# Optimization experiments

Hardware: AMD Instinct MI355X
Metric: run time of the kernel (lower is better)

Reference implementation:

```python
import jax, jax.numpy as jnp
import numpy as np

K, D = 8, 4
LOG2PI = float(np.log(2.0 * np.pi))
TRIL_ROWS, TRIL_COLS = np.tril_indices(D)


def setup_inputs() -> dict:
    key = jax.random.key(0)
    k1, k2 = jax.random.split(key)
    M = 512
    B = 4096
    phi_dim = K + K * D + K * D * (D + 1) // 2  # 120
    phi = jax.random.normal(k1, (M, phi_dim), dtype=jnp.float32)
    X_ref = jax.random.normal(k2, (B, D), dtype=jnp.float32)
    return {"phi": phi, "X_ref": X_ref}


def reference(phi, X_ref):
    M = phi.shape[0]
    B = X_ref.shape[0]
    # unpack_phi: [pi_tilde | mu | L_vecs]
    pi_tilde = phi[:, :K]                                   # [M, K]
    mu = phi[:, K:K + K * D].reshape(M, K, D)               # [M, K, D]
    L_vecs = phi[:, K + K * D:].reshape(M, K, D * (D + 1) // 2)
    # L_vec_to_matrix: lower-triangular fill (row-major tril order)
    L = jnp.zeros((M, K, D, D), phi.dtype).at[:, :, TRIL_ROWS, TRIL_COLS].set(L_vecs)
    pi = jax.nn.softmax(pi_tilde, axis=-1)                  # [M, K]

    # --- mean responsibilities (GMM E-step) ---
    diff = X_ref[None, None, :, :] - mu[:, :, None, :]      # [M, K, B, D]
    L_flat = L.reshape(M * K, D, D)
    diff_flat = jnp.transpose(diff.reshape(M * K, B, D), (0, 2, 1))  # [MK, D, B]
    alpha = jax.scipy.linalg.solve_triangular(L_flat, diff_flat, lower=True)
    maha = (alpha ** 2).sum(1).reshape(M, K, B)             # Mahalanobis distances
    log_det = 2.0 * jnp.log(
        jnp.clip(jnp.abs(jnp.diagonal(L_flat, axis1=-2, axis2=-1)), 1e-8)
    ).sum(-1).reshape(M, K)
    log_norm = -0.5 * (D * LOG2PI + log_det[:, :, None])
    log_gauss = log_norm - 0.5 * maha                       # [M, K, B]
    log_joint = jnp.log(jnp.clip(pi, 1e-8))[:, :, None] + log_gauss
    log_resp = log_joint - jax.scipy.special.logsumexp(log_joint, axis=1, keepdims=True)
    resp = jnp.exp(log_resp).mean(-1)                       # [M, K]

    # --- combined embedding: [mu | log|diag L| | pi | resp] ---
    mu_flat = mu.reshape(M, K * D)
    L_diag = jnp.diagonal(L, axis1=-2, axis2=-1)            # [M, K, D]
    log_L_flat = jnp.log(jnp.clip(jnp.abs(L_diag), 1e-6)).reshape(M, K * D)
    z = jnp.concatenate([mu_flat, log_L_flat, pi, resp], axis=-1)

    # per-feature standardization across particles (torch.std => ddof=1)
    mean = z.mean(axis=0, keepdims=True)
    std = jnp.clip(z.std(axis=0, ddof=1, keepdims=True), 1e-6)
    return (z - mean) / std
```

## Files before the change

kernel.cpp:

```cpp
#include <hip/hip_runtime.h>
#include <math.h>

#define KK 8
#define LOG2E   1.4426950408889634f
#define HL2E    0.7213475204444817f
#define LN2     0.6931471805599453f
#define C2CONST 5.3029936094f
#define L2CLIP8 -26.575424759f


__global__ __launch_bounds__(256) void gmm_setup(const float* __restrict__ phi,
                                                 float* __restrict__ ws,
                                                 float* __restrict__ z) {
    const int tid = blockIdx.x * 256 + threadIdx.x;
    const int m = tid >> 3, k = tid & 7;
    const float* row = phi + m * 120;

    float mx = row[0];
    #pragma unroll
    for (int j = 1; j < KK; ++j) mx = fmaxf(mx, row[j]);
    float s = 0.f;
    #pragma unroll
    for (int j = 0; j < KK; ++j)
        s += __builtin_amdgcn_exp2f((row[j] - mx) * LOG2E);
    float l2s = __builtin_amdgcn_logf(s);
    float pik = __builtin_amdgcn_exp2f((row[k] - mx) * LOG2E) *
                __builtin_amdgcn_rcpf(s);
    float l2pi = fmaxf((row[k] - mx) * LOG2E - l2s, L2CLIP8);

    const float* muk = row + 8 + k * 4;
    const float* Lv  = row + 40 + k * 10;
    float l00 = Lv[0], l10 = Lv[1], l11 = Lv[2], l20 = Lv[3], l21 = Lv[4],
          l22 = Lv[5], l30 = Lv[6], l31 = Lv[7], l32 = Lv[8], l33 = Lv[9];
    float i0 = 1.f / l00, i1 = 1.f / l11, i2 = 1.f / l22, i3 = 1.f / l33;
    float w00 = i0;
    float w10 = -i1 * l10 * w00;
    float w11 = i1;
    float w20 = -i2 * (l20 * w00 + l21 * w10);
    float w21 = -i2 * (l21 * w11);
    float w22 = i2;
    float w30 = -i3 * (l30 * w00 + l31 * w10 + l32 * w20);
    float w31 = -i3 * (l31 * w11 + l32 * w21);
    float w32 = -i3 * (l32 * w22);
    float w33 = i3;
    float sl = __builtin_amdgcn_logf(fmaxf(fabsf(l00), 1e-8f)) +
               __builtin_amdgcn_logf(fmaxf(fabsf(l11), 1e-8f)) +
               __builtin_amdgcn_logf(fmaxf(fabsf(l22), 1e-8f)) +
               __builtin_amdgcn_logf(fmaxf(fabsf(l33), 1e-8f));
    float c2 = l2pi - C2CONST - sl;

    float4* P = reinterpret_cast<float4*>(ws) + tid * 4;
    P[0] = make_float4(muk[0], muk[1], muk[2], muk[3]);
    P[1] = make_float4(w00, w10, w11, w20);
    P[2] = make_float4(w21, w22, w30, w31);
    P[3] = make_float4(w32, w33, c2, 0.f);

    float* zr = z + m * 80;
    #pragma unroll
    for (int d = 0; d < 4; ++d) zr[k * 4 + d] = muk[d];
    zr[32 + k * 4 + 0] = __builtin_amdgcn_logf(fmaxf(fabsf(l00), 1e-6f)) * LN2;
    zr[32 + k * 4 + 1] = __builtin_amdgcn_logf(fmaxf(fabsf(l11), 1e-6f)) * LN2;
    zr[32 + k * 4 + 2] = __builtin_amdgcn_logf(fmaxf(fabsf(l22), 1e-6f)) * LN2;
    zr[32 + k * 4 + 3] = __builtin_amdgcn_logf(fmaxf(fabsf(l33), 1e-6f)) * LN2;
    zr[64 + k] = pik;
}

__global__ __launch_bounds__(256) void gmm_main(const float* __restrict__ ws,
                                                const float* __restrict__ X,
                                                float* __restrict__ part,
                                                int M) {
    const int b = blockIdx.x;
    const int m = b >> 2;
    const int sub = b & 3;
    const int t = threadIdx.x;
    const int w = t >> 6;
    const int lane = t & 63;

    const float4* X4 = reinterpret_cast<const float4*>(X);
    float4 xv[4];
    #pragma unroll
    for (int i = 0; i < 4; ++i)
        xv[i] = X4[sub * 1024 + w * 256 + i * 64 + lane];

    const float4* Pm = reinterpret_cast<const float4*>(ws) + m * 32;

    float acc[KK];
    #pragma unroll
    for (int k = 0; k < KK; ++k) acc[k] = 0.f;

    float lj[4][KK];
    #pragma unroll
    for (int k = 0; k < KK; ++k) {
        float4 p0 = Pm[k * 4 + 0], p1 = Pm[k * 4 + 1],
               p2 = Pm[k * 4 + 2], p3 = Pm[k * 4 + 3];
        #pragma unroll
        for (int i = 0; i < 4; ++i) {
            float d0 = xv[i].x - p0.x;
            float d1 = xv[i].y - p0.y;
            float d2 = xv[i].z - p0.z;
            float d3 = xv[i].w - p0.w;
            float a0 = d0 * p1.x;
            float a1 = fmaf(p1.y, d0, d1 * p1.z);
            float a2 = fmaf(p1.w, d0, fmaf(p2.x, d1, d2 * p2.y));
            float a3 = fmaf(p2.z, d0, fmaf(p2.w, d1, fmaf(p3.x, d2, d3 * p3.y)));
            float sq = fmaf(a0, a0, fmaf(a1, a1, fmaf(a2, a2, a3 * a3)));
            lj[i][k] = fmaf(-HL2E, sq, p3.z);
        }
    }
    #pragma unroll
    for (int i = 0; i < 4; ++i) {
        float mx = lj[i][0];
        #pragma unroll
        for (int k = 1; k < KK; ++k) mx = fmaxf(mx, lj[i][k]);
        float e[KK], s = 0.f;
        #pragma unroll
        for (int k = 0; k < KK; ++k) {
            e[k] = __builtin_amdgcn_exp2f(lj[i][k] - mx);
            s += e[k];
        }
        float inv = __builtin_amdgcn_rcpf(s);
        #pragma unroll
        for (int k = 0; k < KK; ++k) acc[k] = fmaf(e[k], inv, acc[k]);
    }

    #pragma unroll
    for (int k = 0; k < KK; ++k) {
        float v = acc[k];
        #pragma unroll
        for (int off = 32; off; off >>= 1) v += __shfl_xor(v, off, 64);
        acc[k] = v;
    }
    if (lane < KK) {
        int p = sub * 4 + w;
        part[(p * KK + lane) * M + m] = acc[lane];
    }
}

__global__ __launch_bounds__(512) void gmm_norm(const float* __restrict__ part,
                                                float* __restrict__ z, int M) {
    __shared__ float sw[8];
    const int col = blockIdx.x;
    const int t = threadIdx.x;

    float v;
    if (col < 72) {
        v = z[t * 80 + col];
    } else {
        int k = col - 72;
        v = 0.f;
        #pragma unroll
        for (int q = 0; q < 16; ++q) v += part[(q * KK + k) * M + t];
    }

    float r = v;
    #pragma unroll
    for (int off = 32; off; off >>= 1) r += __shfl_xor(r, off, 64);
    if ((t & 63) == 0) sw[t >> 6] = r;
    __syncthreads();
    float tot = 0.f;
    #pragma unroll
    for (int w = 0; w < 8; ++w) tot += sw[w];
    float mean = tot / (float)M;
    __syncthreads();

    float d = v - mean;
    r = d * d;
    #pragma unroll
    for (int off = 32; off; off >>= 1) r += __shfl_xor(r, off, 64);
    if ((t & 63) == 0) sw[t >> 6] = r;
    __syncthreads();
    float tot2 = 0.f;
    #pragma unroll
    for (int w = 0; w < 8; ++w) tot2 += sw[w];
    float stdv = fmaxf(sqrtf(tot2 / (float)(M - 1)), 1e-6f);

    z[t * 80 + col] = d / stdv;
}

extern "C" void kernel_launch(void* const* d_in, const int* in_sizes, int n_in,
                              void* d_out, int out_size, void* d_ws, size_t ws_size,
                              hipStream_t stream) {
    const float* phi = (const float*)d_in[0];
    const float* X   = (const float*)d_in[1];
    const int M = in_sizes[0] / 120;
    float* ws   = (float*)d_ws;
    float* part = ws + 65536;
    float* z    = (float*)d_out;

    gmm_setup<<<(M * KK) / 256, 256, 0, stream>>>(phi, ws, z);
    gmm_main<<<M * 4, 256, 0, stream>>>(ws, X, part, M);
    gmm_norm<<<80, 512, 0, stream>>>(part, z, M);
}
```

Measured before the change: 72.63 us.

## Process all batch points per particle in one block and reduce responsibilities in-block

The main kernel now launches one 256-thread block per particle instead of four. Each block loops over four chunks of the reference points, then reduces the per-wave partial sums through shared memory and writes the responsibility sums straight into the output. This removes the partial-sum buffer and the 16-way gather in the normalization kernel. In exchange the grid shrinks fourfold (512 blocks), which lowers parallelism and latency hiding on a large GPU.

Result: slower. 75.68 us (+4.2%).

```diff
diff --git a/kernel.cpp b/kernel.cpp
--- a/kernel.cpp
+++ b/kernel.cpp
@@ -67,60 +67,60 @@
 
 __global__ __launch_bounds__(256) void gmm_main(const float* __restrict__ ws,
                                                 const float* __restrict__ X,
-                                                float* __restrict__ part,
-                                                int M) {
-    const int b = blockIdx.x;
-    const int m = b >> 2;
-    const int sub = b & 3;
+                                                float* __restrict__ z) {
+    __shared__ float swr[4][KK];
+    const int m = blockIdx.x;
     const int t = threadIdx.x;
     const int w = t >> 6;
     const int lane = t & 63;
 
+    const float4* Pm = reinterpret_cast<const float4*>(ws) + m * 32;
     const float4* X4 = reinterpret_cast<const float4*>(X);
-    float4 xv[4];
-    #pragma unroll
-    for (int i = 0; i < 4; ++i)
-        xv[i] = X4[sub * 1024 + w * 256 + i * 64 + lane];
-
-    const float4* Pm = reinterpret_cast<const float4*>(ws) + m * 32;
 
     float acc[KK];
     #pragma unroll
     for (int k = 0; k < KK; ++k) acc[k] = 0.f;
 
-    float lj[4][KK];
     #pragma unroll
-    for (int k = 0; k < KK; ++k) {
-        float4 p0 = Pm[k * 4 + 0], p1 = Pm[k * 4 + 1],
-               p2 = Pm[k * 4 + 2], p3 = Pm[k * 4 + 3];
+    for (int c = 0; c < 4; ++c) {
+        float4 xv[4];
+        #pragma unroll
+        for (int i = 0; i < 4; ++i) xv[i] = X4[c * 1024 + i * 256 + t];
+
+        float lj[4][KK];
+        #pragma unroll
+        for (int k = 0; k < KK; ++k) {
+            float4 p0 = Pm[k * 4 + 0], p1 = Pm[k * 4 + 1],
+                   p2 = Pm[k * 4 + 2], p3 = Pm[k * 4 + 3];
+            #pragma unroll
+            for (int i = 0; i < 4; ++i) {
+                float d0 = xv[i].x - p0.x;
+                float d1 = xv[i].y - p0.y;
+                float d2 = xv[i].z - p0.z;
+                float d3 = xv[i].w - p0.w;
+                float a0 = d0 * p1.x;
+                float a1 = fmaf(p1.y, d0, d1 * p1.z);
+                float a2 = fmaf(p1.w, d0, fmaf(p2.x, d1, d2 * p2.y));
+                float a3 = fmaf(p2.z, d0, fmaf(p2.w, d1, fmaf(p3.x, d2, d3 * p3.y)));
+                float sq = fmaf(a0, a0, fmaf(a1, a1, fmaf(a2, a2, a3 * a3)));
+                lj[i][k] = fmaf(-HL2E, sq, p3.z);
+            }
+        }
         #pragma unroll
         for (int i = 0; i < 4; ++i) {
-            float d0 = xv[i].x - p0.x;
-            float d1 = xv[i].y - p0.y;
-            float d2 = xv[i].z - p0.z;
-            float d3 = xv[i].w - p0.w;
-            float a0 = d0 * p1.x;
-            float a1 = fmaf(p1.y, d0, d1 * p1.z);
-            float a2 = fmaf(p1.w, d0, fmaf(p2.x, d1, d2 * p2.y));
-            float a3 = fmaf(p2.z, d0, fmaf(p2.w, d1, fmaf(p3.x, d2, d3 * p3.y)));
-            float sq = fmaf(a0, a0, fmaf(a1, a1, fmaf(a2, a2, a3 * a3)));
-            lj[i][k] = fmaf(-HL2E, sq, p3.z);
+            float mx = lj[i][0];
+            #pragma unroll
+            for (int k = 1; k < KK; ++k) mx = fmaxf(mx, lj[i][k]);
+            float e[KK], s = 0.f;
+            #pragma unroll
+            for (int k = 0; k < KK; ++k) {
+                e[k] = __builtin_amdgcn_exp2f(lj[i][k] - mx);
+                s += e[k];
+            }
+            float inv = __builtin_amdgcn_rcpf(s);
+            #pragma unroll
+            for (int k = 0; k < KK; ++k) acc[k] = fmaf(e[k], inv, acc[k]);
         }
-    }
-    #pragma unroll
-    for (int i = 0; i < 4; ++i) {
-        float mx = lj[i][0];
-        #pragma unroll
-        for (int k = 1; k < KK; ++k) mx = fmaxf(mx, lj[i][k]);
-        float e[KK], s = 0.f;
-        #pragma unroll
-        for (int k = 0; k < KK; ++k) {
-            e[k] = __builtin_amdgcn_exp2f(lj[i][k] - mx);
-            s += e[k];
-        }
-        float inv = __builtin_amdgcn_rcpf(s);
-        #pragma unroll
-        for (int k = 0; k < KK; ++k) acc[k] = fmaf(e[k], inv, acc[k]);
     }
 
     #pragma unroll
@@ -130,27 +130,18 @@
         for (int off = 32; off; off >>= 1) v += __shfl_xor(v, off, 64);
         acc[k] = v;
     }
-    if (lane < KK) {
-        int p = sub * 4 + w;
-        part[(p * KK + lane) * M + m] = acc[lane];
-    }
+    if (lane < KK) swr[w][lane] = acc[lane];
+    __syncthreads();
+    if (t < KK)
+        z[m * 80 + 72 + t] = swr[0][t] + swr[1][t] + swr[2][t] + swr[3][t];
 }
 
-__global__ __launch_bounds__(512) void gmm_norm(const float* __restrict__ part,
-                                                float* __restrict__ z, int M) {
+__global__ __launch_bounds__(512) void gmm_norm(float* __restrict__ z, int M) {
     __shared__ float sw[8];
     const int col = blockIdx.x;
     const int t = threadIdx.x;
 
-    float v;
-    if (col < 72) {
-        v = z[t * 80 + col];
-    } else {
-        int k = col - 72;
-        v = 0.f;
-        #pragma unroll
-        for (int q = 0; q < 16; ++q) v += part[(q * KK + k) * M + t];
-    }
+    float v = z[t * 80 + col];
 
     float r = v;
     #pragma unroll
@@ -183,11 +174,10 @@
     const float* phi = (const float*)d_in[0];
     const float* X   = (const float*)d_in[1];
     const int M = in_sizes[0] / 120;
-    float* ws   = (float*)d_ws;
-    float* part = ws + 65536;
-    float* z    = (float*)d_out;
+    float* ws = (float*)d_ws;
+    float* z  = (float*)d_out;
 
     gmm_setup<<<(M * KK) / 256, 256, 0, stream>>>(phi, ws, z);
-    gmm_main<<<M * 4, 256, 0, stream>>>(ws, X, part, M);
-    gmm_norm<<<80, 512, 0, stream>>>(part, z, M);
+    gmm_main<<<M, 256, 0, stream>>>(ws, X, z);
+    gmm_norm<<<80, 512, 0, stream>>>(z, M);
 }
```
